# Performance work log

Hardware: AMD Instinct MI355X
Metric: run time of the kernel (lower is better)

The kernel has to match this reference:

```python
import jax, jax.numpy as jnp
import numpy as np
import math

N = 4096          # num_nodes
E = 128           # embed_dim
H = 8             # num_heads
D = E // H        # head_dim
T = 6             # num_node_types
NE = 65536        # num_edges
ET = 3            # num_edge_types


def setup_inputs() -> dict:
    key = jax.random.key(0)
    ks = jax.random.split(key, 16)
    s = 1.0 / math.sqrt(E)  # xavier-ish scale
    return {
        "query": jax.random.normal(ks[0], (N, E), jnp.float32),
        "key_": jax.random.normal(ks[1], (N, E), jnp.float32),
        "value": jax.random.normal(ks[2], (N, E), jnp.float32),
        # per-type projection weight stacks [T, E, E] (y = x @ W[t] + b[t])
        "Wq": jax.random.normal(ks[3], (T, E, E), jnp.float32) * s,
        "bq": jnp.zeros((T, E), jnp.float32),
        "Wk": jax.random.normal(ks[4], (T, E, E), jnp.float32) * s,
        "bk": jnp.zeros((T, E), jnp.float32),
        "Wv": jax.random.normal(ks[5], (T, E, E), jnp.float32) * s,
        "bv": jnp.zeros((T, E), jnp.float32),
        "edge_bias": jax.random.normal(ks[6], (ET, H), jnp.float32) * 0.1,
        "Wo": jax.random.normal(ks[7], (E, E), jnp.float32) * s,
        "bo": jnp.zeros((E,), jnp.float32),
        "node_types": jax.random.randint(ks[8], (N,), 0, T, jnp.int32),
        "edge_index": jax.random.randint(ks[9], (2, NE), 0, N, jnp.int32),
        "edge_types": jax.random.randint(ks[10], (NE,), 0, ET, jnp.int32),
    }


def _type_proj(x, W, b, node_types):
    # gather per-node weight, batched matvec: [N,E] x [N,E,E] -> [N,E]
    return jnp.einsum("ne,nef->nf", x, W[node_types]) + b[node_types]


def reference(query, key_, value, Wq, bq, Wk, bk, Wv, bv, edge_bias, Wo, bo,
              node_types, edge_index, edge_types):
    Q = _type_proj(query, Wq, bq, node_types).reshape(N, H, D)
    K = _type_proj(key_, Wk, bk, node_types).reshape(N, H, D)
    V = _type_proj(value, Wv, bv, node_types).reshape(N, H, D)

    scores = jnp.einsum("ihd,jhd->hij", Q, K) / math.sqrt(D)  # [H,N,N]

    # edge-type bias: scores[:, tgt, src] += edge_bias[edge_type] (scatter-add, dup-safe)
    src, tgt = edge_index[0], edge_index[1]
    scores = scores.at[:, tgt, src].add(edge_bias[edge_types].T)

    attn = jax.nn.softmax(scores, axis=-1)                    # [H,N,N]
    out = jnp.einsum("hij,jhd->ihd", attn, V).reshape(N, E)
    out = out @ Wo + bo
    return out, attn
```

## Files before the change

### kernel.cpp

```cpp
#include <hip/hip_runtime.h>

static constexpr int kN  = 4096;
static constexpr int kE  = 128;
static constexpr int kH  = 8;
static constexpr int kD  = 16;
static constexpr int kNE = 65536;

typedef float f4 __attribute__((ext_vector_type(4)));

__global__ void proj_kernel(const float* __restrict__ q_in, const float* __restrict__ k_in,
                            const float* __restrict__ v_in,
                            const float* __restrict__ Wq, const float* __restrict__ bq,
                            const float* __restrict__ Wk, const float* __restrict__ bk,
                            const float* __restrict__ Wv, const float* __restrict__ bv,
                            const int* __restrict__ node_types,
                            float* __restrict__ Q, float* __restrict__ K, float* __restrict__ V) {
    const int n = blockIdx.x;
    const int f = threadIdx.x;
    __shared__ float xq[kE], xk[kE], xv[kE];
    xq[f] = q_in[n * kE + f];
    xk[f] = k_in[n * kE + f];
    xv[f] = v_in[n * kE + f];
    __syncthreads();
    const int t = node_types[n];
    const float* wq = Wq + (size_t)t * kE * kE;
    const float* wk = Wk + (size_t)t * kE * kE;
    const float* wv = Wv + (size_t)t * kE * kE;
    float aq = bq[t * kE + f], ak = bk[t * kE + f], av = bv[t * kE + f];
#pragma unroll 8
    for (int e = 0; e < kE; ++e) {
        aq += xq[e] * wq[e * kE + f];
        ak += xk[e] * wk[e * kE + f];
        av += xv[e] * wv[e * kE + f];
    }
    Q[n * kE + f] = aq;
    K[n * kE + f] = ak;
    V[n * kE + f] = av;
}

__global__ void csr_zero_kernel(int* __restrict__ counts) {
    counts[blockIdx.x * 256 + threadIdx.x] = 0;
}

__global__ void csr_count_kernel(const int* __restrict__ edge_index, int* __restrict__ counts) {
    const int e = blockIdx.x * 256 + threadIdx.x;
    atomicAdd(&counts[edge_index[kNE + e]], 1);
}

__global__ void csr_scan_kernel(const int* __restrict__ counts, int* __restrict__ P) {
    __shared__ int buf[1024];
    const int t = threadIdx.x;
    int c[4];
    int s = 0;
#pragma unroll
    for (int u = 0; u < 4; ++u) { c[u] = counts[t * 4 + u]; s += c[u]; }
    buf[t] = s;
    __syncthreads();
    int v = s;
    for (int off = 1; off < 1024; off <<= 1) {
        const int add = (t >= off) ? buf[t - off] : 0;
        __syncthreads();
        v += add;
        buf[t] = v;
        __syncthreads();
    }
    int run = v - s;
#pragma unroll
    for (int u = 0; u < 4; ++u) { P[t * 4 + u] = run; run += c[u]; }
}

__global__ void csr_scatter_kernel(const int* __restrict__ edge_index,
                                   const int* __restrict__ edge_types,
                                   int* __restrict__ P, unsigned short* __restrict__ entries) {
    const int e = blockIdx.x * 256 + threadIdx.x;
    const int src = edge_index[e];
    const int tgt = edge_index[kNE + e];
    const int et  = edge_types[e];
    const int pos = atomicAdd(&P[tgt], 1);
    entries[pos] = (unsigned short)(src | (et << 12));
}

__global__ __launch_bounds__(256, 2) void attn_fused_kernel(
        const float* __restrict__ Q, const float* __restrict__ K, const float* __restrict__ V,
        const int* __restrict__ Pend, const unsigned short* __restrict__ entries,
        const float* __restrict__ edge_bias,
        float* __restrict__ attn, float* __restrict__ OT) {
    const int i0 = blockIdx.x * 4;
    const int h  = blockIdx.y;
    const int t  = threadIdx.x;
    const int w  = t >> 6;
    const int lane = t & 63;
    const int jw = w * 1024;

    __shared__ float S[4][kN];
    __shared__ float ebias_s[3 * kH];
    __shared__ float inv_s[4];
    __shared__ float red[4][64];

    if (t < 3 * kH) ebias_s[t] = edge_bias[t];

    {
        float4 qv[4][4];
#pragma unroll
        for (int r = 0; r < 4; ++r) {
            const float4* qp = (const float4*)(Q + (size_t)(i0 + r) * kE + h * kD);
#pragma unroll
            for (int u = 0; u < 4; ++u) qv[r][u] = qp[u];
        }
#pragma unroll 2
        for (int k = 0; k < 16; ++k) {
            const int j = jw + k * 64 + lane;
            const float4* kp = (const float4*)(K + (size_t)j * kE + h * kD);
            const float4 k0 = kp[0], k1 = kp[1], k2 = kp[2], k3 = kp[3];
#pragma unroll
            for (int r = 0; r < 4; ++r) {
                float a = qv[r][0].x * k0.x + qv[r][0].y * k0.y + qv[r][0].z * k0.z + qv[r][0].w * k0.w;
                a += qv[r][1].x * k1.x + qv[r][1].y * k1.y + qv[r][1].z * k1.z + qv[r][1].w * k1.w;
                a += qv[r][2].x * k2.x + qv[r][2].y * k2.y + qv[r][2].z * k2.z + qv[r][2].w * k2.w;
                a += qv[r][3].x * k3.x + qv[r][3].y * k3.y + qv[r][3].z * k3.z + qv[r][3].w * k3.w;
                S[r][j] = a * 0.25f;
            }
        }
    }
    __syncthreads();

    {
        const int i = i0 + w;
        const int beg = (i == 0) ? 0 : Pend[i - 1];
        const int end = Pend[i];
        for (int idx = beg + lane; idx < end; idx += 64) {
            const unsigned int en = entries[idx];
            atomicAdd(&S[w][en & 0xFFFu], ebias_s[(en >> 12) * kH + h]);
        }
    }
    __syncthreads();

    {
        float4* srow4 = (float4*)&S[w][0];
        float m = -3.4e38f;
#pragma unroll 4
        for (int k = 0; k < 16; ++k) {
            const float4 sv = srow4[k * 64 + lane];
            m = fmaxf(m, fmaxf(fmaxf(sv.x, sv.y), fmaxf(sv.z, sv.w)));
        }
#pragma unroll
        for (int off = 32; off > 0; off >>= 1) m = fmaxf(m, __shfl_xor(m, off, 64));
        float sum = 0.f;
#pragma unroll 2
        for (int k = 0; k < 16; ++k) {
            float4 sv = srow4[k * 64 + lane];
            sv.x = __expf(sv.x - m); sv.y = __expf(sv.y - m);
            sv.z = __expf(sv.z - m); sv.w = __expf(sv.w - m);
            srow4[k * 64 + lane] = sv;
            sum += (sv.x + sv.y) + (sv.z + sv.w);
        }
#pragma unroll
        for (int off = 32; off > 0; off >>= 1) sum += __shfl_xor(sum, off, 64);
        const float inv = 1.f / sum;
        if (lane == 0) inv_s[w] = inv;
        f4* arow = (f4*)(attn + ((size_t)h * kN + (i0 + w)) * kN);
#pragma unroll 2
        for (int k = 0; k < 16; ++k) {
            const float4 ev = srow4[k * 64 + lane];
            f4 pv;
            pv.x = ev.x * inv; pv.y = ev.y * inv; pv.z = ev.z * inv; pv.w = ev.w * inv;
            __builtin_nontemporal_store(pv, &arow[k * 64 + lane]);
        }
    }
    __syncthreads();

    {
        float A[64];
#pragma unroll
        for (int m2 = 0; m2 < 64; ++m2) A[m2] = 0.f;
#pragma unroll 2
        for (int k = 0; k < 16; ++k) {
            const int j = jw + k * 64 + lane;
            const float4* vp = (const float4*)(V + (size_t)j * kE + h * kD);
            const float4 v0 = vp[0], v1 = vp[1], v2 = vp[2], v3 = vp[3];
#pragma unroll
            for (int r = 0; r < 4; ++r) {
                const float s = S[r][j];
                A[r*16+ 0] += s * v0.x; A[r*16+ 1] += s * v0.y; A[r*16+ 2] += s * v0.z; A[r*16+ 3] += s * v0.w;
                A[r*16+ 4] += s * v1.x; A[r*16+ 5] += s * v1.y; A[r*16+ 6] += s * v1.z; A[r*16+ 7] += s * v1.w;
                A[r*16+ 8] += s * v2.x; A[r*16+ 9] += s * v2.y; A[r*16+10] += s * v2.z; A[r*16+11] += s * v2.w;
                A[r*16+12] += s * v3.x; A[r*16+13] += s * v3.y; A[r*16+14] += s * v3.z; A[r*16+15] += s * v3.w;
            }
        }
#define FOLD(OFF, HALF)                                                   \
        {                                                                 \
            const bool hi = (lane & OFF) != 0;                            \
            _Pragma("unroll")                                             \
            for (int i2 = 0; i2 < HALF; ++i2) {                           \
                const float a = A[i2], b = A[i2 + HALF];                  \
                float keep = hi ? b : a;                                  \
                const float send = hi ? a : b;                            \
                keep += __shfl_xor(send, OFF, 64);                        \
                A[i2] = keep;                                             \
            }                                                             \
        }
        FOLD(32, 32) FOLD(16, 16) FOLD(8, 8) FOLD(4, 4) FOLD(2, 2) FOLD(1, 1)
#undef FOLD
        red[w][lane] = A[0];
    }
    __syncthreads();
    if (t < 64) {
        const int r = t >> 4, d = t & 15;
        const float v = (red[0][t] + red[1][t] + red[2][t] + red[3][t]) * inv_s[r];
        OT[(size_t)(i0 + r) * kE + h * kD + d] = v;
    }
}

__global__ void out_proj_kernel(const float* __restrict__ OT, const float* __restrict__ Wo,
                                const float* __restrict__ bo, float* __restrict__ out) {
    const int n = blockIdx.x, f = threadIdx.x;
    __shared__ float x[kE];
    x[f] = OT[n * kE + f];
    __syncthreads();
    float a = bo[f];
#pragma unroll 8
    for (int e = 0; e < kE; ++e) a += x[e] * Wo[e * kE + f];
    out[n * kE + f] = a;
}

extern "C" void kernel_launch(void* const* d_in, const int* in_sizes, int n_in,
                              void* d_out, int out_size, void* d_ws, size_t ws_size,
                              hipStream_t stream) {
    const float* query = (const float*)d_in[0];
    const float* key_  = (const float*)d_in[1];
    const float* value = (const float*)d_in[2];
    const float* Wq    = (const float*)d_in[3];
    const float* bq    = (const float*)d_in[4];
    const float* Wk    = (const float*)d_in[5];
    const float* bk    = (const float*)d_in[6];
    const float* Wv    = (const float*)d_in[7];
    const float* bv    = (const float*)d_in[8];
    const float* ebias = (const float*)d_in[9];
    const float* Wo    = (const float*)d_in[10];
    const float* bo    = (const float*)d_in[11];
    const int* node_types = (const int*)d_in[12];
    const int* edge_index = (const int*)d_in[13];
    const int* edge_types = (const int*)d_in[14];

    float* out  = (float*)d_out;
    float* attn = (float*)d_out + (size_t)kN * kE;

    float* ws = (float*)d_ws;
    float* Q = ws;
    float* K = ws + (size_t)kN * kE;
    float* V = ws + 2 * (size_t)kN * kE;
    int* counts = (int*)(ws + 3 * (size_t)kN * kE);
    int* P      = counts + kN;
    unsigned short* entries = (unsigned short*)(P + kN);
    float* OT = out;

    proj_kernel<<<kN, kE, 0, stream>>>(query, key_, value, Wq, bq, Wk, bk, Wv, bv,
                                       node_types, Q, K, V);
    csr_zero_kernel<<<kN / 256, 256, 0, stream>>>(counts);
    csr_count_kernel<<<kNE / 256, 256, 0, stream>>>(edge_index, counts);
    csr_scan_kernel<<<1, 1024, 0, stream>>>(counts, P);
    csr_scatter_kernel<<<kNE / 256, 256, 0, stream>>>(edge_index, edge_types, P, entries);
    attn_fused_kernel<<<dim3(kN / 4, kH), 256, 0, stream>>>(Q, K, V, P, entries, ebias,
                                                            attn, OT);
    out_proj_kernel<<<kN, kE, 0, stream>>>(OT, Wo, bo, out);
}
```

Measured before the change: 1.016 ms.

## Double attention block threads, split softmax rows across wave pairs, prefetch K/V

The fused attention kernel now runs 512 threads per block, so each wave covers 512 columns instead of 1024. Softmax max and sum for each row are split across two waves and combined through shared memory, which adds a barrier. The normalized attn store moves into the P·V loop, which drops a separate pass over the row. K and V loads are software-pipelined with next-iteration prefetch, and the counts zeroing is folded into the projection kernel to save one launch. The risks are higher register pressure from the 512,4 launch bounds and the extra synchronization.

```diff
diff --git a/kernel.cpp b/kernel.cpp
--- a/kernel.cpp
+++ b/kernel.cpp
@@ -14,9 +14,11 @@
                             const float* __restrict__ Wk, const float* __restrict__ bk,
                             const float* __restrict__ Wv, const float* __restrict__ bv,
                             const int* __restrict__ node_types,
-                            float* __restrict__ Q, float* __restrict__ K, float* __restrict__ V) {
+                            float* __restrict__ Q, float* __restrict__ K, float* __restrict__ V,
+                            int* __restrict__ counts) {
     const int n = blockIdx.x;
     const int f = threadIdx.x;
+    if (f == 0) counts[n] = 0;
     __shared__ float xq[kE], xk[kE], xv[kE];
     xq[f] = q_in[n * kE + f];
     xk[f] = k_in[n * kE + f];
@@ -38,10 +40,6 @@
     V[n * kE + f] = av;
 }
 
-__global__ void csr_zero_kernel(int* __restrict__ counts) {
-    counts[blockIdx.x * 256 + threadIdx.x] = 0;
-}
-
 __global__ void csr_count_kernel(const int* __restrict__ edge_index, int* __restrict__ counts) {
     const int e = blockIdx.x * 256 + threadIdx.x;
     atomicAdd(&counts[edge_index[kNE + e]], 1);
@@ -80,7 +78,7 @@
     entries[pos] = (unsigned short)(src | (et << 12));
 }
 
-__global__ __launch_bounds__(256, 2) void attn_fused_kernel(
+__global__ __launch_bounds__(512, 4) void attn_fused_kernel(
         const float* __restrict__ Q, const float* __restrict__ K, const float* __restrict__ V,
         const int* __restrict__ Pend, const unsigned short* __restrict__ entries,
         const float* __restrict__ edge_bias,
@@ -90,12 +88,13 @@
     const int t  = threadIdx.x;
     const int w  = t >> 6;
     const int lane = t & 63;
-    const int jw = w * 1024;
+    const int jw = w * 512;
 
     __shared__ float S[4][kN];
     __shared__ float ebias_s[3 * kH];
-    __shared__ float inv_s[4];
-    __shared__ float red[4][64];
+    __shared__ float pmax[4][2];
+    __shared__ float psum[4][2];
+    __shared__ float red[8][64];
 
     if (t < 3 * kH) ebias_s[t] = edge_bias[t];
 
@@ -107,85 +106,128 @@
 #pragma unroll
             for (int u = 0; u < 4; ++u) qv[r][u] = qp[u];
         }
-#pragma unroll 2
-        for (int k = 0; k < 16; ++k) {
+        const float* kb = K + (size_t)(jw + lane) * kE + h * kD;
+        float4 kc[4], kn[4];
+        {
+            const float4* kp = (const float4*)kb;
+#pragma unroll
+            for (int u = 0; u < 4; ++u) kc[u] = kp[u];
+        }
+#pragma unroll
+        for (int k = 0; k < 8; ++k) {
+            if (k < 7) {
+                const float4* kp = (const float4*)(kb + (size_t)(k + 1) * 64 * kE);
+#pragma unroll
+                for (int u = 0; u < 4; ++u) kn[u] = kp[u];
+            }
             const int j = jw + k * 64 + lane;
-            const float4* kp = (const float4*)(K + (size_t)j * kE + h * kD);
-            const float4 k0 = kp[0], k1 = kp[1], k2 = kp[2], k3 = kp[3];
 #pragma unroll
             for (int r = 0; r < 4; ++r) {
-                float a = qv[r][0].x * k0.x + qv[r][0].y * k0.y + qv[r][0].z * k0.z + qv[r][0].w * k0.w;
-                a += qv[r][1].x * k1.x + qv[r][1].y * k1.y + qv[r][1].z * k1.z + qv[r][1].w * k1.w;
-                a += qv[r][2].x * k2.x + qv[r][2].y * k2.y + qv[r][2].z * k2.z + qv[r][2].w * k2.w;
-                a += qv[r][3].x * k3.x + qv[r][3].y * k3.y + qv[r][3].z * k3.z + qv[r][3].w * k3.w;
+                float a = qv[r][0].x * kc[0].x + qv[r][0].y * kc[0].y + qv[r][0].z * kc[0].z + qv[r][0].w * kc[0].w;
+                a += qv[r][1].x * kc[1].x + qv[r][1].y * kc[1].y + qv[r][1].z * kc[1].z + qv[r][1].w * kc[1].w;
+                a += qv[r][2].x * kc[2].x + qv[r][2].y * kc[2].y + qv[r][2].z * kc[2].z + qv[r][2].w * kc[2].w;
+                a += qv[r][3].x * kc[3].x + qv[r][3].y * kc[3].y + qv[r][3].z * kc[3].z + qv[r][3].w * kc[3].w;
                 S[r][j] = a * 0.25f;
             }
-        }
-    }
-    __syncthreads();
-
-    {
-        const int i = i0 + w;
+#pragma unroll
+            for (int u = 0; u < 4; ++u) kc[u] = kn[u];
+        }
+    }
+    __syncthreads();
+
+    {
+        const int r = w >> 1;
+        const int i = i0 + r;
         const int beg = (i == 0) ? 0 : Pend[i - 1];
         const int end = Pend[i];
-        for (int idx = beg + lane; idx < end; idx += 64) {
+        for (int idx = beg + (w & 1) * 64 + lane; idx < end; idx += 128) {
             const unsigned int en = entries[idx];
-            atomicAdd(&S[w][en & 0xFFFu], ebias_s[(en >> 12) * kH + h]);
-        }
-    }
-    __syncthreads();
-
-    {
-        float4* srow4 = (float4*)&S[w][0];
+            atomicAdd(&S[r][en & 0xFFFu], ebias_s[(en >> 12) * kH + h]);
+        }
+    }
+    __syncthreads();
+
+    {
+        const int r = w >> 1, hf = w & 1;
+        const float4* srow4 = (const float4*)&S[r][0];
+        const int base = hf * 512;
         float m = -3.4e38f;
-#pragma unroll 4
-        for (int k = 0; k < 16; ++k) {
-            const float4 sv = srow4[k * 64 + lane];
+#pragma unroll
+        for (int kk = 0; kk < 8; ++kk) {
+            const float4 sv = srow4[base + kk * 64 + lane];
             m = fmaxf(m, fmaxf(fmaxf(sv.x, sv.y), fmaxf(sv.z, sv.w)));
         }
 #pragma unroll
         for (int off = 32; off > 0; off >>= 1) m = fmaxf(m, __shfl_xor(m, off, 64));
+        if (lane == 0) pmax[r][hf] = m;
+    }
+    __syncthreads();
+
+    {
+        const int r = w >> 1, hf = w & 1;
+        float4* srow4 = (float4*)&S[r][0];
+        const int base = hf * 512;
+        const float m = fmaxf(pmax[r][0], pmax[r][1]);
         float sum = 0.f;
 #pragma unroll 2
-        for (int k = 0; k < 16; ++k) {
-            float4 sv = srow4[k * 64 + lane];
+        for (int kk = 0; kk < 8; ++kk) {
+            float4 sv = srow4[base + kk * 64 + lane];
             sv.x = __expf(sv.x - m); sv.y = __expf(sv.y - m);
             sv.z = __expf(sv.z - m); sv.w = __expf(sv.w - m);
-            srow4[k * 64 + lane] = sv;
+            srow4[base + kk * 64 + lane] = sv;
             sum += (sv.x + sv.y) + (sv.z + sv.w);
         }
 #pragma unroll
         for (int off = 32; off > 0; off >>= 1) sum += __shfl_xor(sum, off, 64);
-        const float inv = 1.f / sum;
-        if (lane == 0) inv_s[w] = inv;
-        f4* arow = (f4*)(attn + ((size_t)h * kN + (i0 + w)) * kN);
-#pragma unroll 2
-        for (int k = 0; k < 16; ++k) {
-            const float4 ev = srow4[k * 64 + lane];
-            f4 pv;
-            pv.x = ev.x * inv; pv.y = ev.y * inv; pv.z = ev.z * inv; pv.w = ev.w * inv;
-            __builtin_nontemporal_store(pv, &arow[k * 64 + lane]);
-        }
-    }
-    __syncthreads();
-
-    {
+        if (lane == 0) psum[r][hf] = sum;
+    }
+    __syncthreads();
+
+    {
+        float invr[4];
+#pragma unroll
+        for (int r = 0; r < 4; ++r) invr[r] = 1.f / (psum[r][0] + psum[r][1]);
+
         float A[64];
 #pragma unroll
         for (int m2 = 0; m2 < 64; ++m2) A[m2] = 0.f;
-#pragma unroll 2
-        for (int k = 0; k < 16; ++k) {
+
+        const float* vb = V + (size_t)(jw + lane) * kE + h * kD;
+        float* abase = attn + ((size_t)h * kN + i0) * kN;
+        float4 vc[4], vn[4];
+        float sc[4], sn[4];
+        {
+            const float4* vp = (const float4*)vb;
+#pragma unroll
+            for (int u = 0; u < 4; ++u) vc[u] = vp[u];
+#pragma unroll
+            for (int r = 0; r < 4; ++r) sc[r] = S[r][jw + lane];
+        }
+#pragma unroll
+        for (int k = 0; k < 8; ++k) {
             const int j = jw + k * 64 + lane;
-            const float4* vp = (const float4*)(V + (size_t)j * kE + h * kD);
-            const float4 v0 = vp[0], v1 = vp[1], v2 = vp[2], v3 = vp[3];
+            if (k < 7) {
+                const float4* vp = (const float4*)(vb + (size_t)(k + 1) * 64 * kE);
+#pragma unroll
+                for (int u = 0; u < 4; ++u) vn[u] = vp[u];
+#pragma unroll
+                for (int r = 0; r < 4; ++r) sn[r] = S[r][j + 64];
+            }
+#pragma unroll
+            for (int r = 0; r < 4; ++r)
+                __builtin_nontemporal_store(sc[r] * invr[r], abase + (size_t)r * kN + j);
 #pragma unroll
             for (int r = 0; r < 4; ++r) {
-                const float s = S[r][j];
-                A[r*16+ 0] += s * v0.x; A[r*16+ 1] += s * v0.y; A[r*16+ 2] += s * v0.z; A[r*16+ 3] += s * v0.w;
-                A[r*16+ 4] += s * v1.x; A[r*16+ 5] += s * v1.y; A[r*16+ 6] += s * v1.z; A[r*16+ 7] += s * v1.w;
-                A[r*16+ 8] += s * v2.x; A[r*16+ 9] += s * v2.y; A[r*16+10] += s * v2.z; A[r*16+11] += s * v2.w;
-                A[r*16+12] += s * v3.x; A[r*16+13] += s * v3.y; A[r*16+14] += s * v3.z; A[r*16+15] += s * v3.w;
+                const float s = sc[r];
+                A[r*16+ 0] += s * vc[0].x; A[r*16+ 1] += s * vc[0].y; A[r*16+ 2] += s * vc[0].z; A[r*16+ 3] += s * vc[0].w;
+                A[r*16+ 4] += s * vc[1].x; A[r*16+ 5] += s * vc[1].y; A[r*16+ 6] += s * vc[1].z; A[r*16+ 7] += s * vc[1].w;
+                A[r*16+ 8] += s * vc[2].x; A[r*16+ 9] += s * vc[2].y; A[r*16+10] += s * vc[2].z; A[r*16+11] += s * vc[2].w;
+                A[r*16+12] += s * vc[3].x; A[r*16+13] += s * vc[3].y; A[r*16+14] += s * vc[3].z; A[r*16+15] += s * vc[3].w;
             }
+#pragma unroll
+            for (int u = 0; u < 4; ++u) vc[u] = vn[u];
+#pragma unroll
+            for (int r = 0; r < 4; ++r) sc[r] = sn[r];
         }
 #define FOLD(OFF, HALF)                                                   \
         {                                                                 \
@@ -206,8 +248,11 @@
     __syncthreads();
     if (t < 64) {
         const int r = t >> 4, d = t & 15;
-        const float v = (red[0][t] + red[1][t] + red[2][t] + red[3][t]) * inv_s[r];
-        OT[(size_t)(i0 + r) * kE + h * kD + d] = v;
+        float acc = 0.f;
+#pragma unroll
+        for (int u = 0; u < 8; ++u) acc += red[u][t];
+        const float inv = 1.f / (psum[r][0] + psum[r][1]);
+        OT[(size_t)(i0 + r) * kE + h * kD + d] = acc * inv;
     }
 }
 
@@ -255,12 +300,11 @@
     float* OT = out;
 
     proj_kernel<<<kN, kE, 0, stream>>>(query, key_, value, Wq, bq, Wk, bk, Wv, bv,
-                                       node_types, Q, K, V);
-    csr_zero_kernel<<<kN / 256, 256, 0, stream>>>(counts);
+                                       node_types, Q, K, V, counts);
     csr_count_kernel<<<kNE / 256, 256, 0, stream>>>(edge_index, counts);
     csr_scan_kernel<<<1, 1024, 0, stream>>>(counts, P);
     csr_scatter_kernel<<<kNE / 256, 256, 0, stream>>>(edge_index, edge_types, P, entries);
-    attn_fused_kernel<<<dim3(kN / 4, kH), 256, 0, stream>>>(Q, K, V, P, entries, ebias,
+    attn_fused_kernel<<<dim3(kN / 4, kH), 512, 0, stream>>>(Q, K, V, P, entries, ebias,
                                                             attn, OT);
     out_proj_kernel<<<kN, kE, 0, stream>>>(OT, Wo, bo, out);
 }
```

After: 1.143 ms. 1.12x slower.
